# Kernel optimization log

Measured on AMD Instinct MI355X. Metric: run time of the kernel, lower is better.

The kernel has to match this reference:

```python
import jax, jax.numpy as jnp
import numpy as np

N, L, D_MODEL, N_HEADS = 2, 2048, 512, 8

def setup_inputs() -> dict:
    key = jax.random.key(0)
    x = jax.random.normal(key, (N, L, D_MODEL), dtype=jnp.float32)
    return {"input_data": x}

def reference(input_data):
    n, l, _ = input_data.shape
    h = N_HEADS
    d = D_MODEL // h  # head dim
    # Q = K = V = reshaped input (the Linear projections are unused in the original forward)
    q = input_data.reshape(n, l, h, d)
    k = q
    v = q
    scale = 1.0 / jnp.sqrt(jnp.float32(d))
    # scores: [n, h, l, s]
    scores = jnp.einsum('nlhd,nshd->nhls', q, k)
    attn_weights = jax.nn.softmax(scale * scores, axis=-1)
    # updated values: [n, l, h, d]
    updated_v = jnp.einsum('nhls,nshd->nlhd', attn_weights, v)
    out = updated_v.reshape(n, l, h * d)
    # attn returned as mean over heads: permute nhls -> nlhs, mean over h -> [n, l, s]
    attn = jnp.transpose(attn_weights, (0, 2, 1, 3)).mean(axis=-2)
    return (out, attn)
```

## Files before the change

kernel.cpp:

```cpp
#include <hip/hip_runtime.h>

#define NBATCH 2
#define SEQ    2048
#define DMODEL 512
#define NH     8
#define HDIM   64
#define SCALE  0.125f

#define K2 0.1803368801111204f

#if __has_builtin(__builtin_amdgcn_exp2f)
#define EXP2(x) __builtin_amdgcn_exp2f(x)
#else
#define EXP2(x) __expf((x) * 0.6931471805599453f)
#endif

typedef __attribute__((ext_vector_type(8)))  short bf16x8;
typedef __attribute__((ext_vector_type(4)))  float f32x4;
typedef __attribute__((ext_vector_type(16))) float f32x16;

__device__ __forceinline__ unsigned short f2bf(float f) {
    union { float f; unsigned u; } v; v.f = f;
    unsigned r = v.u + 0x7FFFu + ((v.u >> 16) & 1u);
    return (unsigned short)(r >> 16);
}

__device__ __forceinline__ void pack4(unsigned short* dst, float4 v) {
    unsigned long long pk = (unsigned long long)f2bf(v.x)
        | ((unsigned long long)f2bf(v.y) << 16)
        | ((unsigned long long)f2bf(v.z) << 32)
        | ((unsigned long long)f2bf(v.w) << 48);
    __builtin_memcpy(dst, &pk, 8);
}

__device__ __forceinline__ bf16x8 pack8(float4 a, float4 b) {
    bf16x8 r;
    r[0]=(short)f2bf(a.x); r[1]=(short)f2bf(a.y); r[2]=(short)f2bf(a.z); r[3]=(short)f2bf(a.w);
    r[4]=(short)f2bf(b.x); r[5]=(short)f2bf(b.y); r[6]=(short)f2bf(b.z); r[7]=(short)f2bf(b.w);
    return r;
}

__device__ __forceinline__ unsigned cvt_pk_bf16(float s0, float s1) {
    unsigned d;
    asm("v_cvt_pk_bf16_f32 %0, %1, %2" : "=v"(d) : "v"(s0), "v"(s1));
    return d;
}

__device__ __forceinline__ void gld_lds16(const unsigned short* g, unsigned short* l) {
    __builtin_amdgcn_global_load_lds(
        (const __attribute__((address_space(1))) unsigned int*)(const void*)g,
        (__attribute__((address_space(3))) unsigned int*)(void*)l, 16, 0, 0);
}

__global__ __launch_bounds__(256) void prep_kernel(const float* __restrict__ x,
                                                   unsigned short* __restrict__ xb,
                                                   unsigned short* __restrict__ xt) {
    __shared__ unsigned short Tb[64][72];
    const int bid = blockIdx.x;
    const int n = bid >> 8, h = (bid >> 5) & 7, st = bid & 31;
    const int s0 = st * 64;
    const int t = threadIdx.x;
    {
        const int s = t >> 2, d0 = (t & 3) * 16;
        const float* xp = x + ((size_t)(n*SEQ + s0 + s))*DMODEL + h*HDIM + d0;
        #pragma unroll
        for (int i = 0; i < 4; ++i) pack4(&Tb[s][d0 + 4*i], *(const float4*)(xp + 4*i));
    }
    __syncthreads();
    {
        const int s = t >> 2, d0 = (t & 3) * 16;
        unsigned short* bp = xb + ((size_t)(n*SEQ + s0 + s))*DMODEL + h*HDIM + d0;
        *(bf16x8*)bp       = *(const bf16x8*)&Tb[s][d0];
        *(bf16x8*)(bp + 8) = *(const bf16x8*)&Tb[s][d0 + 8];
    }
    {
        const int d = t >> 2, c0 = (t & 3) * 16;
        bf16x8 v0, v1;
        #pragma unroll
        for (int j = 0; j < 8; ++j) {
            v0[j] = (short)Tb[c0 + j][d];
            v1[j] = (short)Tb[c0 + 8 + j][d];
        }
        unsigned short* tp = xt + ((size_t)((n*NH + h)*HDIM + d))*SEQ + s0 + c0;
        *(bf16x8*)tp       = v0;
        *(bf16x8*)(tp + 8) = v1;
    }
}

__global__ __launch_bounds__(256, 4) void out_kernel5(const unsigned short* __restrict__ xb,
                                                      const unsigned short* __restrict__ xt,
                                                      float* __restrict__ out,
                                                      float* __restrict__ rho,
                                                      float* __restrict__ part,
                                                      int split) {
    __shared__ unsigned short Kb[2][64*64];
    __shared__ unsigned short Vt[2][64*64];

    const int i   = blockIdx.x;
    const int cps = gridDim.x >> 3;
    const int bid = (i & 7) * cps + (i >> 3);
    int n, h, lt, ss;
    if (split) { n = bid >> 9; h = (bid >> 6) & 7; lt = (bid >> 1) & 31; ss = bid & 1; }
    else       { n = bid >> 8; h = (bid >> 5) & 7; lt = bid & 31;        ss = 0;       }
    const int l0 = lt * 64;
    const int sbase = ss << 10;
    const int nch = split ? 16 : 32;

    const int tid = threadIdx.x;
    const int wv = tid >> 6, lane = tid & 63;
    const int lrow = lane & 31;
    const int hi = lane >> 5;
    const int qh = wv & 1, sh = wv >> 1;

    const unsigned short* qg = xb + ((size_t)(n*SEQ + l0 + qh*32 + lrow))*DMODEL + h*HDIM;
    bf16x8 qf[4];
    #pragma unroll
    for (int kst = 0; kst < 4; ++kst)
        qf[kst] = *(const bf16x8*)(qg + kst*16 + hi*8);

    const int srow8  = wv*8 + (lane >> 3);
    const int schunk = lane & 7;
    const unsigned short* kbase = xb + (size_t)(n*SEQ)*DMODEL + h*HDIM;
    const unsigned short* vbase = xt + ((size_t)(n*NH + h)*HDIM)*SEQ;

    auto stage = [&](int buf, int s0) {
        #pragma unroll
        for (int it = 0; it < 2; ++it) {
            const int row = it*32 + srow8;
            const int gc  = schunk ^ (row & 7);
            gld_lds16(kbase + (size_t)(s0 + row)*DMODEL + gc*8,
                      &Kb[buf][it*2048 + wv*512]);
        }
        #pragma unroll
        for (int it = 0; it < 2; ++it) {
            const int d  = it*32 + srow8;
            const int gc = schunk ^ (d & 7);
            gld_lds16(vbase + (size_t)d*SEQ + s0 + gc*8,
                      &Vt[buf][it*2048 + wv*512]);
        }
    };

    f32x16 ovA = {0.f}, ovB = {0.f};
    #pragma unroll
    for (int r = 0; r < 16; ++r) { ovA[r] = 0.f; ovB[r] = 0.f; }
    float rs = 0.f;

    stage(0, sbase);
    __syncthreads();
    int cur = 0;

    for (int c = 0; c < nch; ++c) {
        if (c < nch - 1) stage(cur ^ 1, sbase + (c + 1) * 64);

        f32x16 acc;
        #pragma unroll
        for (int r = 0; r < 16; ++r) acc[r] = 0.f;
        #pragma unroll
        for (int kst = 0; kst < 4; ++kst) {
            const int g = ((kst*2 + hi) ^ (lrow & 7)) << 3;
            const bf16x8 kf = *(const bf16x8*)&Kb[cur][(sh*32 + lrow)*64 + g];
            acc = __builtin_amdgcn_mfma_f32_32x32x16_bf16(kf, qf[kst], acc, 0, 0, 0);
        }
        #pragma unroll
        for (int r = 0; r < 16; ++r) {
            acc[r] = EXP2(acc[r] * K2);
            rs += acc[r];
        }
        #pragma unroll
        for (int p = 0; p < 2; ++p) {
            const unsigned g0 = cvt_pk_bf16(acc[8*p+0], acc[8*p+1]);
            const unsigned g1 = cvt_pk_bf16(acc[8*p+2], acc[8*p+3]);
            const unsigned g2 = cvt_pk_bf16(acc[8*p+4], acc[8*p+5]);
            const unsigned g3 = cvt_pk_bf16(acc[8*p+6], acc[8*p+7]);
            const unsigned b0 = hi ? g0 : g2;
            const unsigned b1 = hi ? g1 : g3;
            const unsigned r0 = (unsigned)__shfl_xor((int)b0, 32);
            const unsigned r1 = (unsigned)__shfl_xor((int)b1, 32);
            union { unsigned u[4]; bf16x8 h8; } pf;
            pf.u[0] = hi ? r0 : g0;
            pf.u[1] = hi ? r1 : g1;
            pf.u[2] = hi ? g2 : r0;
            pf.u[3] = hi ? g3 : r1;
            const int gv = ((sh*4 + p*2 + hi) ^ (lrow & 7)) << 3;
            const bf16x8 v0 = *(const bf16x8*)&Vt[cur][( 0 + lrow)*64 + gv];
            const bf16x8 v1 = *(const bf16x8*)&Vt[cur][(32 + lrow)*64 + gv];
            ovA = __builtin_amdgcn_mfma_f32_32x32x16_bf16(v0, pf.h8, ovA, 0, 0, 0);
            ovB = __builtin_amdgcn_mfma_f32_32x32x16_bf16(v1, pf.h8, ovB, 0, 0, 0);
        }
        __syncthreads();
        cur ^= 1;
    }

    rs += __shfl_xor(rs, 32);
    float* red = (float*)&Vt[0][0];
    float* rsr = (float*)&Kb[0][0];
    if (sh == 1) {
        #pragma unroll
        for (int g = 0; g < 4; ++g) {
            float4 a = { ovA[4*g+0], ovA[4*g+1], ovA[4*g+2], ovA[4*g+3] };
            float4 b = { ovB[4*g+0], ovB[4*g+1], ovB[4*g+2], ovB[4*g+3] };
            *(float4*)&red[qh*2048 + lrow*64 +  0 + g*8 + 4*hi] = a;
            *(float4*)&red[qh*2048 + lrow*64 + 32 + g*8 + 4*hi] = b;
        }
        if (hi == 0) rsr[qh*32 + lrow] = rs;
    }
    __syncthreads();
    if (sh == 0) {
        const float rs_tot = rs + rsr[qh*32 + lrow];
        #pragma unroll
        for (int g = 0; g < 4; ++g) {
            float4 a = *(const float4*)&red[qh*2048 + lrow*64 +  0 + g*8 + 4*hi];
            float4 b = *(const float4*)&red[qh*2048 + lrow*64 + 32 + g*8 + 4*hi];
            ovA[4*g+0]+=a.x; ovA[4*g+1]+=a.y; ovA[4*g+2]+=a.z; ovA[4*g+3]+=a.w;
            ovB[4*g+0]+=b.x; ovB[4*g+1]+=b.y; ovB[4*g+2]+=b.z; ovB[4*g+3]+=b.w;
        }
        const int qloc = qh*32 + lrow;
        if (split) {
            float* pp = part + ((size_t)(((n*NH + h)*32 + lt)*2 + ss))*4160;
            #pragma unroll
            for (int g = 0; g < 4; ++g) {
                float4 a = { ovA[4*g+0], ovA[4*g+1], ovA[4*g+2], ovA[4*g+3] };
                float4 b = { ovB[4*g+0], ovB[4*g+1], ovB[4*g+2], ovB[4*g+3] };
                *(float4*)&pp[qloc*64 +  0 + g*8 + 4*hi] = a;
                *(float4*)&pp[qloc*64 + 32 + g*8 + 4*hi] = b;
            }
            if (hi == 0) pp[4096 + qloc] = rs_tot;
        } else {
            const float iv = 1.f / rs_tot;
            float* op = out + ((size_t)(n*SEQ + l0 + qloc))*DMODEL + h*HDIM;
            #pragma unroll
            for (int g = 0; g < 4; ++g) {
                float4 a = { ovA[4*g+0]*iv, ovA[4*g+1]*iv, ovA[4*g+2]*iv, ovA[4*g+3]*iv };
                float4 b = { ovB[4*g+0]*iv, ovB[4*g+1]*iv, ovB[4*g+2]*iv, ovB[4*g+3]*iv };
                *(float4*)&op[ 0 + g*8 + 4*hi] = a;
                *(float4*)&op[32 + g*8 + 4*hi] = b;
            }
            if (hi == 0) rho[(size_t)(n*NH + h)*SEQ + l0 + qloc] = rs_tot;
        }
    }
}

__global__ __launch_bounds__(256) void combine_kernel(const float* __restrict__ part,
                                                      float* __restrict__ out,
                                                      float* __restrict__ rho) {
    const int bid = blockIdx.x;
    const int n = bid >> 8, h = (bid >> 5) & 7, lt = bid & 31;
    const int l0 = lt * 64;
    const int tid = threadIdx.x;
    const int q = tid >> 2, dg = (tid & 3) * 16;

    const float* p0 = part + ((size_t)(((n*NH + h)*32 + lt)*2))*4160;
    const float* p1 = p0 + 4160;
    const float rs = p0[4096 + q] + p1[4096 + q];
    const float iv = 1.f / rs;
    if ((tid & 3) == 0)
        rho[(size_t)(n*NH + h)*SEQ + l0 + q] = rs;

    float* op = out + ((size_t)(n*SEQ + l0 + q))*DMODEL + h*HDIM + dg;
    #pragma unroll
    for (int i = 0; i < 4; ++i) {
        float4 a = *(const float4*)&p0[q*64 + dg + 4*i];
        float4 b = *(const float4*)&p1[q*64 + dg + 4*i];
        float4 o = { (a.x+b.x)*iv, (a.y+b.y)*iv, (a.z+b.z)*iv, (a.w+b.w)*iv };
        *(float4*)&op[4*i] = o;
    }
}

__global__ __launch_bounds__(256) void mean_kernel4(const unsigned short* __restrict__ xb,
                                                    const float* __restrict__ rho,
                                                    float* __restrict__ attn) {
    __shared__ unsigned short Qb[2][64*64];
    __shared__ unsigned short Kb[2][64*64];
    __shared__ float invb[NH][64];

    const int i   = blockIdx.x;
    const int bid = (i & 7) * 256 + (i >> 3);
    const int n = bid >> 10, lt = (bid >> 5) & 31, st = bid & 31;
    const int l0 = lt * 64, s0 = st * 64;
    const int tid = threadIdx.x;
    const int wv = tid >> 6, lane = tid & 63;
    const int lr = lane & 15, lg = lane >> 4;

    for (int j = tid; j < NH*64; j += 256) {
        const int hh = j >> 6, row = j & 63;
        invb[hh][row] = 0.125f / rho[(size_t)(n*NH + hh)*SEQ + l0 + row];
    }

    const int srow8  = wv*8 + (lane >> 3);
    const int schunk = lane & 7;

    auto stage = [&](int buf, int h) {
        #pragma unroll
        for (int it = 0; it < 2; ++it) {
            const int row = it*32 + srow8;
            const int gc  = schunk ^ (row & 7);
            gld_lds16(xb + ((size_t)(n*SEQ + l0 + row))*DMODEL + h*HDIM + gc*8,
                      &Qb[buf][it*2048 + wv*512]);
        }
        #pragma unroll
        for (int it = 0; it < 2; ++it) {
            const int row = it*32 + srow8;
            const int gc  = schunk ^ (row & 7);
            gld_lds16(xb + ((size_t)(n*SEQ + s0 + row))*DMODEL + h*HDIM + gc*8,
                      &Kb[buf][it*2048 + wv*512]);
        }
    };

    float mean[4][4];
    #pragma unroll
    for (int ct = 0; ct < 4; ++ct)
        #pragma unroll
        for (int r = 0; r < 4; ++r) mean[ct][r] = 0.f;

    stage(0, 0);
    __syncthreads();
    int cur = 0;

    for (int h = 0; h < NH; ++h) {
        if (h < NH-1) stage(cur ^ 1, h + 1);

        const int qrow = wv*16 + lr;
        const int c0 = (lg ^ (lr & 7)) << 3;
        const bf16x8 a0 = *(const bf16x8*)&Qb[cur][qrow*64 + c0];
        const bf16x8 a1 = *(const bf16x8*)&Qb[cur][qrow*64 + (c0 ^ 32)];
        const float logiv = __log2f(invb[h][wv*16 + lr]);
        #pragma unroll
        for (int ct = 0; ct < 4; ++ct) {
            const unsigned short* kr = &Kb[cur][(ct*16 + lr)*64];
            bf16x8 b0 = *(const bf16x8*)&kr[c0];
            bf16x8 b1 = *(const bf16x8*)&kr[c0 ^ 32];
            f32x4 acc = {0.f,0.f,0.f,0.f};
            acc = __builtin_amdgcn_mfma_f32_16x16x32_bf16(b0, a0, acc, 0,0,0);
            acc = __builtin_amdgcn_mfma_f32_16x16x32_bf16(b1, a1, acc, 0,0,0);
            #pragma unroll
            for (int r = 0; r < 4; ++r)
                mean[ct][r] += EXP2(fmaf(acc[r], K2, logiv));
        }
        __syncthreads();
        cur ^= 1;
    }

    const int arow = n*SEQ + l0 + wv*16 + lr;
    #pragma unroll
    for (int ct = 0; ct < 4; ++ct) {
        float4 v = { mean[ct][0], mean[ct][1], mean[ct][2], mean[ct][3] };
        *(float4*)&attn[(size_t)arow*SEQ + s0 + ct*16 + lg*4] = v;
    }
}

__global__ __launch_bounds__(256) void fb_out_kernel(const float* __restrict__ x,
                                                     float* __restrict__ out,
                                                     float* __restrict__ rho) {
    __shared__ unsigned short Kbuf[128][72];
    __shared__ unsigned short vT[64][136];
    __shared__ unsigned short pbuf[64][136];
    const int bid = blockIdx.x;
    const int n  = bid >> 8, h = (bid >> 5) & 7, lt = bid & 31;
    const int l0 = lt * 64;
    const int tid = threadIdx.x;
    const int wv  = tid >> 6, lane = tid & 63;
    const int lr  = lane & 15, lg = lane >> 4;
    const float* qp = x + ((size_t)(n*SEQ + l0 + wv*16 + lr))*DMODEL + h*HDIM + lg*8;
    const bf16x8 a0 = pack8(*(const float4*)qp,      *(const float4*)(qp+4));
    const bf16x8 a1 = pack8(*(const float4*)(qp+32), *(const float4*)(qp+36));
    f32x4 ov0 = {0.f,0.f,0.f,0.f}, ov1 = {0.f,0.f,0.f,0.f};
    f32x4 ov2 = {0.f,0.f,0.f,0.f}, ov3 = {0.f,0.f,0.f,0.f};
    float rs[4] = {0.f,0.f,0.f,0.f};
    for (int s0 = 0; s0 < SEQ; s0 += 128) {
        __syncthreads();
        {
            const int srow = tid >> 1, dbase = (tid & 1) * 32;
            const float* kp = x + ((size_t)(n*SEQ + s0 + srow))*DMODEL + h*HDIM + dbase;
            #pragma unroll
            for (int i = 0; i < 8; ++i) {
                float4 v = *(const float4*)(kp + 4*i);
                pack4(&Kbuf[srow][dbase + 4*i], v);
                const int d = dbase + 4*i;
                vT[d+0][srow] = f2bf(v.x); vT[d+1][srow] = f2bf(v.y);
                vT[d+2][srow] = f2bf(v.z); vT[d+3][srow] = f2bf(v.w);
            }
        }
        __syncthreads();
        #pragma unroll
        for (int ct = 0; ct < 8; ++ct) {
            const unsigned short* bp = &Kbuf[ct*16 + lr][lg*8];
            bf16x8 b0 = *(const bf16x8*)bp;
            bf16x8 b1 = *(const bf16x8*)(bp + 32);
            f32x4 acc = {0.f,0.f,0.f,0.f};
            acc = __builtin_amdgcn_mfma_f32_16x16x32_bf16(a0, b0, acc, 0,0,0);
            acc = __builtin_amdgcn_mfma_f32_16x16x32_bf16(a1, b1, acc, 0,0,0);
            #pragma unroll
            for (int r = 0; r < 4; ++r) {
                const float e = __expf(acc[r] * SCALE);
                rs[r] += e;
                pbuf[wv*16 + lg*4 + r][ct*16 + lr] = f2bf(e);
            }
        }
        __syncthreads();
        #pragma unroll
        for (int ks = 0; ks < 4; ++ks) {
            bf16x8 pa = *(const bf16x8*)&pbuf[wv*16 + lr][ks*32 + lg*8];
            bf16x8 v0 = *(const bf16x8*)&vT[ 0 + lr][ks*32 + lg*8];
            bf16x8 v1 = *(const bf16x8*)&vT[16 + lr][ks*32 + lg*8];
            bf16x8 v2 = *(const bf16x8*)&vT[32 + lr][ks*32 + lg*8];
            bf16x8 v3 = *(const bf16x8*)&vT[48 + lr][ks*32 + lg*8];
            ov0 = __builtin_amdgcn_mfma_f32_16x16x32_bf16(pa, v0, ov0, 0,0,0);
            ov1 = __builtin_amdgcn_mfma_f32_16x16x32_bf16(pa, v1, ov1, 0,0,0);
            ov2 = __builtin_amdgcn_mfma_f32_16x16x32_bf16(pa, v2, ov2, 0,0,0);
            ov3 = __builtin_amdgcn_mfma_f32_16x16x32_bf16(pa, v3, ov3, 0,0,0);
        }
    }
    #pragma unroll
    for (int r = 0; r < 4; ++r) {
        float s = rs[r];
        s += __shfl_xor(s, 1, 16); s += __shfl_xor(s, 2, 16);
        s += __shfl_xor(s, 4, 16); s += __shfl_xor(s, 8, 16);
        rs[r] = s;
    }
    const int row0 = l0 + wv*16 + lg*4;
    if (lr == 0) {
        #pragma unroll
        for (int r = 0; r < 4; ++r)
            rho[(size_t)(n*NH + h)*SEQ + row0 + r] = rs[r];
    }
    #pragma unroll
    for (int r = 0; r < 4; ++r) {
        const float iv = 1.f / rs[r];
        float* op = out + ((size_t)(n*SEQ + row0 + r))*DMODEL + h*HDIM + lr;
        op[0] = ov0[r]*iv; op[16] = ov1[r]*iv; op[32] = ov2[r]*iv; op[48] = ov3[r]*iv;
    }
}

__global__ __launch_bounds__(256) void fb_mean_kernel(const float* __restrict__ x,
                                                      const float* __restrict__ rho,
                                                      float* __restrict__ attn) {
    __shared__ unsigned short Qb[64][72];
    __shared__ unsigned short Kb[128][72];
    __shared__ float          invb[64];
    const int bid = blockIdx.x;
    const int n  = bid >> 9, lt = (bid >> 4) & 31, st = bid & 15;
    const int l0 = lt * 64, s0 = st * 128;
    const int tid = threadIdx.x;
    const int wv  = tid >> 6, lane = tid & 63;
    const int lr  = lane & 15, lg = lane >> 4;
    float mean[8][4];
    #pragma unroll
    for (int ct = 0; ct < 8; ++ct)
        #pragma unroll
        for (int r = 0; r < 4; ++r) mean[ct][r] = 0.f;
    for (int h = 0; h < NH; ++h) {
        __syncthreads();
        {
            const int qrow = tid >> 2, qd = (tid & 3) * 16;
            const float* qp = x + ((size_t)(n*SEQ + l0 + qrow))*DMODEL + h*HDIM + qd;
            #pragma unroll
            for (int i = 0; i < 4; ++i)
                pack4(&Qb[qrow][qd + 4*i], *(const float4*)(qp + 4*i));
        }
        {
            const int srow = tid >> 1, dbase = (tid & 1) * 32;
            const float* kp = x + ((size_t)(n*SEQ + s0 + srow))*DMODEL + h*HDIM + dbase;
            #pragma unroll
            for (int i = 0; i < 8; ++i)
                pack4(&Kb[srow][dbase + 4*i], *(const float4*)(kp + 4*i));
        }
        if (tid < 64)
            invb[tid] = 0.125f / rho[(size_t)(n*NH + h)*SEQ + l0 + tid];
        __syncthreads();
        const unsigned short* ap = &Qb[wv*16 + lr][lg*8];
        const bf16x8 a0 = *(const bf16x8*)ap;
        const bf16x8 a1 = *(const bf16x8*)(ap + 32);
        #pragma unroll
        for (int ct = 0; ct < 8; ++ct) {
            const unsigned short* bp = &Kb[ct*16 + lr][lg*8];
            bf16x8 b0 = *(const bf16x8*)bp;
            bf16x8 b1 = *(const bf16x8*)(bp + 32);
            f32x4 acc = {0.f,0.f,0.f,0.f};
            acc = __builtin_amdgcn_mfma_f32_16x16x32_bf16(a0, b0, acc, 0,0,0);
            acc = __builtin_amdgcn_mfma_f32_16x16x32_bf16(a1, b1, acc, 0,0,0);
            #pragma unroll
            for (int r = 0; r < 4; ++r)
                mean[ct][r] += __expf(acc[r] * SCALE) * invb[wv*16 + lg*4 + r];
        }
    }
    #pragma unroll
    for (int ct = 0; ct < 8; ++ct)
        #pragma unroll
        for (int r = 0; r < 4; ++r)
            attn[((size_t)(n*SEQ + l0 + wv*16 + lg*4 + r))*SEQ + s0 + ct*16 + lr]
                = mean[ct][r];
}

extern "C" void kernel_launch(void* const* d_in, const int* in_sizes, int n_in,
                              void* d_out, int out_size, void* d_ws, size_t ws_size,
                              hipStream_t stream) {
    (void)in_sizes; (void)n_in; (void)out_size;
    const float* x = (const float*)d_in[0];
    float* out  = (float*)d_out;
    float* attn = out + (size_t)NBATCH*SEQ*DMODEL;
    float* rho  = (float*)d_ws;

    const size_t XB_OFF   = 131072;
    const size_t XT_OFF   = XB_OFF + 4194304;
    const size_t NEED1    = XT_OFF + 4194304;
    const size_t PART_OFF = NEED1;
    const size_t NEED2    = PART_OFF + (size_t)1024*4160*4;

    if (ws_size >= NEED1) {
        unsigned short* xb = (unsigned short*)((char*)d_ws + XB_OFF);
        unsigned short* xt = (unsigned short*)((char*)d_ws + XT_OFF);
        prep_kernel <<<dim3(512),  dim3(256), 0, stream>>>(x, xb, xt);
        if (ws_size >= NEED2) {
            float* part = (float*)((char*)d_ws + PART_OFF);
            out_kernel5   <<<dim3(1024), dim3(256), 0, stream>>>(xb, xt, out, rho, part, 1);
            combine_kernel<<<dim3(512),  dim3(256), 0, stream>>>(part, out, rho);
        } else {
            out_kernel5   <<<dim3(512),  dim3(256), 0, stream>>>(xb, xt, out, rho, nullptr, 0);
        }
        mean_kernel4<<<dim3(2048), dim3(256), 0, stream>>>(xb, rho, attn);
    } else {
        fb_out_kernel <<<dim3(512),  dim3(256), 0, stream>>>(x, out, rho);
        fb_mean_kernel<<<dim3(1024), dim3(256), 0, stream>>>(x, rho, attn);
    }
}
```

Baseline: 77.60 us.

## Fuse split-K combine into mean kernel and read Q fragments directly from global

```diff
diff --git a/kernel.cpp b/kernel.cpp
--- a/kernel.cpp
+++ b/kernel.cpp
@@ -240,36 +240,11 @@
     }
 }
 
-__global__ __launch_bounds__(256) void combine_kernel(const float* __restrict__ part,
-                                                      float* __restrict__ out,
-                                                      float* __restrict__ rho) {
-    const int bid = blockIdx.x;
-    const int n = bid >> 8, h = (bid >> 5) & 7, lt = bid & 31;
-    const int l0 = lt * 64;
-    const int tid = threadIdx.x;
-    const int q = tid >> 2, dg = (tid & 3) * 16;
-
-    const float* p0 = part + ((size_t)(((n*NH + h)*32 + lt)*2))*4160;
-    const float* p1 = p0 + 4160;
-    const float rs = p0[4096 + q] + p1[4096 + q];
-    const float iv = 1.f / rs;
-    if ((tid & 3) == 0)
-        rho[(size_t)(n*NH + h)*SEQ + l0 + q] = rs;
-
-    float* op = out + ((size_t)(n*SEQ + l0 + q))*DMODEL + h*HDIM + dg;
-    #pragma unroll
-    for (int i = 0; i < 4; ++i) {
-        float4 a = *(const float4*)&p0[q*64 + dg + 4*i];
-        float4 b = *(const float4*)&p1[q*64 + dg + 4*i];
-        float4 o = { (a.x+b.x)*iv, (a.y+b.y)*iv, (a.z+b.z)*iv, (a.w+b.w)*iv };
-        *(float4*)&op[4*i] = o;
-    }
-}
-
-__global__ __launch_bounds__(256) void mean_kernel4(const unsigned short* __restrict__ xb,
+__global__ __launch_bounds__(256) void mean_kernel5(const unsigned short* __restrict__ xb,
                                                     const float* __restrict__ rho,
+                                                    const float* __restrict__ part,
+                                                    float* __restrict__ out,
                                                     float* __restrict__ attn) {
-    __shared__ unsigned short Qb[2][64*64];
     __shared__ unsigned short Kb[2][64*64];
     __shared__ float invb[NH][64];
 
@@ -281,22 +256,10 @@
     const int wv = tid >> 6, lane = tid & 63;
     const int lr = lane & 15, lg = lane >> 4;
 
-    for (int j = tid; j < NH*64; j += 256) {
-        const int hh = j >> 6, row = j & 63;
-        invb[hh][row] = 0.125f / rho[(size_t)(n*NH + hh)*SEQ + l0 + row];
-    }
-
     const int srow8  = wv*8 + (lane >> 3);
     const int schunk = lane & 7;
 
     auto stage = [&](int buf, int h) {
-        #pragma unroll
-        for (int it = 0; it < 2; ++it) {
-            const int row = it*32 + srow8;
-            const int gc  = schunk ^ (row & 7);
-            gld_lds16(xb + ((size_t)(n*SEQ + l0 + row))*DMODEL + h*HDIM + gc*8,
-                      &Qb[buf][it*2048 + wv*512]);
-        }
         #pragma unroll
         for (int it = 0; it < 2; ++it) {
             const int row = it*32 + srow8;
@@ -306,24 +269,56 @@
         }
     };
 
+    stage(0, 0);
+
+    if (part != nullptr && st < NH) {
+        const int hC = st;
+        const float* p0 = part + ((size_t)(((n*NH + hC)*32 + lt)*2))*4160;
+        const float* p1 = p0 + 4160;
+        const int q = tid >> 2, dg = (tid & 3) * 16;
+        const float rsT = p0[4096 + q] + p1[4096 + q];
+        const float iv = 1.f / rsT;
+        float* op = out + ((size_t)(n*SEQ + l0 + q))*DMODEL + hC*HDIM + dg;
+        #pragma unroll
+        for (int k = 0; k < 4; ++k) {
+            float4 a = *(const float4*)&p0[q*64 + dg + 4*k];
+            float4 b = *(const float4*)&p1[q*64 + dg + 4*k];
+            float4 o = { (a.x+b.x)*iv, (a.y+b.y)*iv, (a.z+b.z)*iv, (a.w+b.w)*iv };
+            *(float4*)&op[4*k] = o;
+        }
+    }
+
+    for (int j = tid; j < NH*64; j += 256) {
+        const int hh = j >> 6, row = j & 63;
+        float rv;
+        if (part != nullptr) {
+            const float* pb_ = part + ((size_t)(((n*NH + hh)*32 + lt)*2))*4160 + 4096;
+            rv = pb_[row] + pb_[4160 + row];
+        } else {
+            rv = rho[(size_t)(n*NH + hh)*SEQ + l0 + row];
+        }
+        invb[hh][row] = 0.125f / rv;
+    }
+
     float mean[4][4];
     #pragma unroll
     for (int ct = 0; ct < 4; ++ct)
         #pragma unroll
         for (int r = 0; r < 4; ++r) mean[ct][r] = 0.f;
 
-    stage(0, 0);
     __syncthreads();
     int cur = 0;
 
+    const int qrow = wv*16 + lr;
+    const unsigned short* qg = xb + ((size_t)(n*SEQ + l0 + qrow))*DMODEL;
+
     for (int h = 0; h < NH; ++h) {
         if (h < NH-1) stage(cur ^ 1, h + 1);
 
-        const int qrow = wv*16 + lr;
+        const bf16x8 a0 = *(const bf16x8*)(qg + h*HDIM + lg*8);
+        const bf16x8 a1 = *(const bf16x8*)(qg + h*HDIM + 32 + lg*8);
+        const float logiv = __log2f(invb[h][qrow]);
         const int c0 = (lg ^ (lr & 7)) << 3;
-        const bf16x8 a0 = *(const bf16x8*)&Qb[cur][qrow*64 + c0];
-        const bf16x8 a1 = *(const bf16x8*)&Qb[cur][qrow*64 + (c0 ^ 32)];
-        const float logiv = __log2f(invb[h][wv*16 + lr]);
         #pragma unroll
         for (int ct = 0; ct < 4; ++ct) {
             const unsigned short* kr = &Kb[cur][(ct*16 + lr)*64];
@@ -340,7 +335,7 @@
         cur ^= 1;
     }
 
-    const int arow = n*SEQ + l0 + wv*16 + lr;
+    const int arow = n*SEQ + l0 + qrow;
     #pragma unroll
     for (int ct = 0; ct < 4; ++ct) {
         float4 v = { mean[ct][0], mean[ct][1], mean[ct][2], mean[ct][3] };
@@ -512,12 +507,12 @@
         prep_kernel <<<dim3(512),  dim3(256), 0, stream>>>(x, xb, xt);
         if (ws_size >= NEED2) {
             float* part = (float*)((char*)d_ws + PART_OFF);
-            out_kernel5   <<<dim3(1024), dim3(256), 0, stream>>>(xb, xt, out, rho, part, 1);
-            combine_kernel<<<dim3(512),  dim3(256), 0, stream>>>(part, out, rho);
+            out_kernel5 <<<dim3(1024), dim3(256), 0, stream>>>(xb, xt, out, rho, part, 1);
+            mean_kernel5<<<dim3(2048), dim3(256), 0, stream>>>(xb, rho, part, out, attn);
         } else {
-            out_kernel5   <<<dim3(512),  dim3(256), 0, stream>>>(xb, xt, out, rho, nullptr, 0);
-        }
-        mean_kernel4<<<dim3(2048), dim3(256), 0, stream>>>(xb, rho, attn);
+            out_kernel5 <<<dim3(512),  dim3(256), 0, stream>>>(xb, xt, out, rho, nullptr, 0);
+            mean_kernel5<<<dim3(2048), dim3(256), 0, stream>>>(xb, rho, nullptr, out, attn);
+        }
     } else {
         fb_out_kernel <<<dim3(512),  dim3(256), 0, stream>>>(x, out, rho);
         fb_mean_kernel<<<dim3(1024), dim3(256), 0, stream>>>(x, rho, attn);
```

New measurement: 79.97 us. +3.1%, slower.
